# Performance work log

Hardware: AMD Instinct MI355X
Metric: run time of the kernel (lower is better)

The kernel has to match this reference:

```python
import jax, jax.numpy as jnp
import numpy as np

B, LQ, LA, H = 32, 1024, 1024, 512
NEG = -1e7


def setup_inputs() -> dict:
    key = jax.random.key(0)
    kq, ka, ku = jax.random.split(key, 3)
    q = jax.random.normal(kq, (B, LQ, H), dtype=jnp.float32)
    a = jax.random.normal(ka, (B, LA, H), dtype=jnp.float32)
    U = 0.02 * jax.random.normal(ku, (H, H), dtype=jnp.float32)  # init.normal(std=0.02)
    q_mask = jnp.ones((B, LQ, 1), dtype=jnp.float32)
    a_mask = jnp.ones((B, LA, 1), dtype=jnp.float32)
    return {"q": q, "a": a, "U": U, "q_mask": q_mask, "a_mask": a_mask}


def reference(q, a, U, q_mask, a_mask):
    # mask[b,i,j] = q_mask[b,i] * a_mask[b,j]  (nonzero => valid)
    mask = jnp.matmul(q_mask, jnp.swapaxes(a_mask, 1, 2)) > 0  # [B,LQ,LA] bool
    # bilinear score X = q @ U @ a^T
    qU = jnp.einsum('bqh,hk->bqk', q, U)
    X = jnp.einsum('bqk,bak->bqa', qU, a)  # [B,LQ,LA]
    X = jnp.where(mask, X, NEG)
    I = jax.nn.sigmoid(X)
    att_a2q = jnp.max(jax.nn.softmax(I, axis=-1), axis=-1)  # [B,LQ]
    att_q2a = jnp.max(jax.nn.softmax(I, axis=-2), axis=-2)  # [B,LA]
    q_attn = jnp.einsum('blh,bl->bh', q, att_a2q)  # [B,H]
    a_attn = jnp.einsum('blh,bl->bh', a, att_q2a)  # [B,H]
    return q_attn, a_attn
```

## Files before the change

kernel.cpp:

```cpp
#include <hip/hip_runtime.h>

typedef __attribute__((ext_vector_type(8))) short bf16x8;
typedef __attribute__((ext_vector_type(4))) float f32x4;
typedef unsigned short u16;
typedef unsigned int u32;

#define NLOG2E -1.44269504088896f
#define LOG2E   1.44269504088896f
#define SLICE 32768

__device__ __forceinline__ float bf2f(u16 x) {
  union { u32 u; float f; } v; v.u = ((u32)x) << 16; return v.f;
}
__device__ __forceinline__ u16 f2b(float f) {
  union { float f; u32 u; } v; v.f = f;
  return (u16)((v.u + 0x7FFFu + ((v.u >> 16) & 1u)) >> 16);
}
__device__ __forceinline__ u32 pk2(float lo, float hi) {
  return (u32)f2b(lo) | ((u32)f2b(hi) << 16);
}
__device__ __forceinline__ bool inputs_are_bf16(const void* qmask) {
  return *(const u32*)qmask == 0x3F803F80u;
}

__global__ __launch_bounds__(256) void prep_all(
    const void* __restrict__ q, const void* __restrict__ a,
    const void* __restrict__ U, const void* __restrict__ qmask,
    u16* __restrict__ qb, u16* __restrict__ ab, u16* __restrict__ Ut,
    float* __restrict__ out)
{
  const bool bf = inputs_are_bf16(qmask);
  const int t = threadIdx.x;
  if (blockIdx.x < 8192) {
    const bool isq = blockIdx.x < 4096;
    const int idx = (isq ? blockIdx.x : blockIdx.x - 4096) * 256 + t;
    const void* src = isq ? q : a;
    u16* dst = isq ? qb : ab;
    if (bf) {
      const bf16x8* s = (const bf16x8*)src;
      bf16x8* d = (bf16x8*)dst;
      d[idx * 2]     = s[idx * 2];
      d[idx * 2 + 1] = s[idx * 2 + 1];
    } else {
      const float4* s = (const float4*)src + (size_t)idx * 4;
      float4 v0 = s[0], v1 = s[1], v2 = s[2], v3 = s[3];
      uint4* d = (uint4*)dst + (size_t)idx * 2;
      uint4 w0, w1;
      w0.x = pk2(v0.x, v0.y); w0.y = pk2(v0.z, v0.w);
      w0.z = pk2(v1.x, v1.y); w0.w = pk2(v1.z, v1.w);
      w1.x = pk2(v2.x, v2.y); w1.y = pk2(v2.z, v2.w);
      w1.z = pk2(v3.x, v3.y); w1.w = pk2(v3.z, v3.w);
      d[0] = w0;
      d[1] = w1;
    }
  } else {
    const int bb = blockIdx.x - 8192;
    out[bb * 512 + t] = 0.f;
    out[bb * 512 + 256 + t] = 0.f;
    __shared__ u16 tile[64][65];
    const int bx = bb & 7, by = bb >> 3;
    #pragma unroll
    for (int i = 0; i < 16; i++) {
      int r = i * 4 + (t >> 6);
      int c = t & 63;
      size_t gi = (size_t)(by * 64 + r) * 512 + bx * 64 + c;
      tile[c][r] = bf ? ((const u16*)U)[gi] : f2b(((const float*)U)[gi]);
    }
    __syncthreads();
    #pragma unroll
    for (int i = 0; i < 16; i++) {
      int r = i * 4 + (t >> 6);
      int c = t & 63;
      Ut[(size_t)(bx * 64 + r) * 512 + by * 64 + c] = tile[r][c];
    }
  }
}

template<int EPI>
__global__ __launch_bounds__(256, 2) void gemm_bt(
    const u16* __restrict__ A, const u16* __restrict__ B,
    u16* __restrict__ C, float scaleC,
    size_t strideA, size_t strideB,
    const void* __restrict__ q_mask, const void* __restrict__ a_mask,
    float* __restrict__ statsP)
{
  __shared__ __align__(16) char smem[66560];
  u16* As0 = (u16*)smem;
  u16* Bs0 = (u16*)(smem + 16384);
  u16* As1 = (u16*)(smem + 32768);
  u16* Bs1 = (u16*)(smem + 49152);
  u16* Ct  = (u16*)smem;
  float* redS = (float*)smem;
  float* redM = (float*)(smem + 16896);
  float* colS = (float*)(smem + 33792);
  float* colM = (float*)(smem + 34816);
  float* qp = (float*)(smem + 65536);
  float* ap = (float*)(smem + 66048);

  const int bx = blockIdx.x, by = blockIdx.y, bz = blockIdx.z;
  const int tid  = threadIdx.x;
  const int lane = tid & 63;
  const int wave = tid >> 6;
  const int wr = wave >> 1, wc = wave & 1;
  const int l15 = lane & 15, lq = lane >> 4;
  const int rsub = lane >> 3;
  const int csw  = (lane & 7) ^ rsub;

  const u16* Ab = A + strideA * bz + (size_t)by * 128 * 512;
  const u16* Bb = B + strideB * bz + (size_t)bx * 128 * 512;

  if (EPI) {
    const bool bf = inputs_are_bf16(q_mask);
    if (tid < 128) {
      int gi = bz * 1024 + by * 128 + tid;
      float v = bf ? bf2f(((const u16*)q_mask)[gi]) : ((const float*)q_mask)[gi];
      qp[tid] = (v > 0.f) ? 0.f : 1e30f;
    } else {
      int gj = bz * 1024 + bx * 128 + (tid - 128);
      float v = bf ? bf2f(((const u16*)a_mask)[gj]) : ((const float*)a_mask)[gj];
      ap[tid - 128] = (v > 0.f) ? 0.f : 1e30f;
    }
    __syncthreads();
  }

  f32x4 acc[4][4];
  if (EPI) {
    #pragma unroll
    for (int mt = 0; mt < 4; mt++)
      #pragma unroll
      for (int nt = 0; nt < 4; nt++) {
        float cp = ap[wc * 64 + nt * 16 + l15];
        #pragma unroll
        for (int r = 0; r < 4; r++)
          acc[mt][nt][r] = qp[wr * 64 + mt * 16 + lq * 4 + r] + cp;
      }
  } else {
    #pragma unroll
    for (int i = 0; i < 4; i++)
      #pragma unroll
      for (int j = 0; j < 4; j++) {
        f32x4 z = {0.f, 0.f, 0.f, 0.f};
        acc[i][j] = z;
      }
  }

  auto stage = [&](u16* Asb, u16* Bsb, int k0) {
    #pragma unroll
    for (int i = 0; i < 4; i++) {
      const int r0 = wave * 32 + i * 8;
      const size_t go = (size_t)(r0 + rsub) * 512 + k0 + csw * 8;
      __builtin_amdgcn_global_load_lds(
          (const __attribute__((address_space(1))) void*)(Ab + go),
          (__attribute__((address_space(3))) void*)&Asb[r0 * 64], 16, 0, 0);
      __builtin_amdgcn_global_load_lds(
          (const __attribute__((address_space(1))) void*)(Bb + go),
          (__attribute__((address_space(3))) void*)&Bsb[r0 * 64], 16, 0, 0);
    }
  };

  stage(As0, Bs0, 0);
  #pragma unroll
  for (int t = 0; t < 8; t++) {
    u16* Asc = (t & 1) ? As1 : As0;
    u16* Bsc = (t & 1) ? Bs1 : Bs0;
    if (t < 7) {
      stage((t & 1) ? As0 : As1, (t & 1) ? Bs0 : Bs1, (t + 1) * 64);
      asm volatile("s_waitcnt vmcnt(8)\n\ts_barrier" ::: "memory");
    } else {
      asm volatile("s_waitcnt vmcnt(0)\n\ts_barrier" ::: "memory");
    }
    #pragma unroll
    for (int ks = 0; ks < 64; ks += 32) {
      const int cx = ((ks >> 3) + lq) ^ (l15 & 7);
      bf16x8 af[4], bfr[4];
      #pragma unroll
      for (int tt = 0; tt < 4; tt++) {
        af[tt]  = *(const bf16x8*)&Asc[(wr * 64 + tt * 16 + l15) * 64 + cx * 8];
        bfr[tt] = *(const bf16x8*)&Bsc[(wc * 64 + tt * 16 + l15) * 64 + cx * 8];
      }
      #pragma unroll
      for (int mt = 0; mt < 4; mt++)
        #pragma unroll
        for (int nt = 0; nt < 4; nt++)
          acc[mt][nt] = __builtin_amdgcn_mfma_f32_16x16x32_bf16(af[mt], bfr[nt], acc[mt][nt], 0, 0, 0);
    }
    asm volatile("s_waitcnt lgkmcnt(0)\n\ts_barrier" ::: "memory");
  }

  if (!EPI) {
    #pragma unroll
    for (int mt = 0; mt < 4; mt++)
      #pragma unroll
      for (int nt = 0; nt < 4; nt++)
        #pragma unroll
        for (int r = 0; r < 4; r++) {
          int row = wr * 64 + mt * 16 + lq * 4 + r;
          int col = wc * 64 + nt * 16 + l15;
          Ct[row * 144 + col] = f2b(scaleC * acc[mt][nt][r]);
        }
    __syncthreads();
    u16* Cb = C + (size_t)by * 128 * 512 + bx * 128;
    #pragma unroll
    for (int i = 0; i < 8; i++) {
      int c = tid + i * 256;
      int row = c >> 4, cc = c & 15;
      *(bf16x8*)&Cb[(size_t)row * 512 + cc * 8] = *(const bf16x8*)&Ct[row * 144 + cc * 8];
    }
  } else {
    const int gi0 = bz * 1024 + by * 128;
    const int gj0 = bz * 1024 + bx * 128;
    float* rowsumP = statsP + 0      + bx * SLICE;
    float* colsumP = statsP + 262144 + by * SLICE;
    float* rowminP = statsP + 524288 + bx * SLICE;
    float* colminP = statsP + 786432 + by * SLICE;

    float csum[4] = {0.f, 0.f, 0.f, 0.f};
    float cmin[4] = {3e38f, 3e38f, 3e38f, 3e38f};
    #pragma unroll
    for (int mt = 0; mt < 4; mt++) {
      #pragma unroll
      for (int r = 0; r < 4; r++) {
        const int row = wr * 64 + mt * 16 + lq * 4 + r;
        float rsm = 0.f, rmn = 3e38f;
        #pragma unroll
        for (int nt = 0; nt < 4; nt++) {
          float y = acc[mt][nt][r];
          float u = __builtin_amdgcn_exp2f(y);
          float s = __builtin_amdgcn_rcpf(1.f + u);
          float e = __builtin_amdgcn_exp2f(LOG2E * s);
          rsm += e;
          csum[nt] += e;
          rmn = fminf(rmn, y);
          cmin[nt] = fminf(cmin[nt], y);
        }
        redS[row * 33 + l15 + 16 * wc] = rsm;
        redM[row * 33 + l15 + 16 * wc] = rmn;
      }
    }
    #pragma unroll
    for (int nt = 0; nt < 4; nt++) {
      float cs = csum[nt], cm = cmin[nt];
      cs += __shfl_xor(cs, 16); cm = fminf(cm, __shfl_xor(cm, 16));
      cs += __shfl_xor(cs, 32); cm = fminf(cm, __shfl_xor(cm, 32));
      if (lane < 16) {
        int j = wc * 64 + nt * 16 + l15;
        colS[j * 2 + wr] = cs;
        colM[j * 2 + wr] = cm;
      }
    }
    __syncthreads();
    if (tid < 128) {
      float s = 0.f;
      #pragma unroll
      for (int j = 0; j < 32; j++) s += redS[tid * 33 + j];
      rowsumP[gi0 + tid] = s;
      colsumP[gj0 + tid] = colS[tid * 2] + colS[tid * 2 + 1];
    } else {
      const int r = tid - 128;
      float m = 3e38f;
      #pragma unroll
      for (int j = 0; j < 32; j++) m = fminf(m, redM[r * 33 + j]);
      rowminP[gi0 + r] = m;
      colminP[gj0 + r] = fminf(colM[r * 2], colM[r * 2 + 1]);
    }
  }
}

__global__ __launch_bounds__(256) void partial_kernel(
    const u16* __restrict__ qb, const u16* __restrict__ ab,
    const float* __restrict__ statsP, float* __restrict__ out)
{
  __shared__ float att[128];
  const int tid = threadIdx.x;
  const int seg = blockIdx.x;
  const int b = blockIdx.y >> 1, half = blockIdx.y & 1;
  if (tid < 128) {
    const int g = b * 1024 + seg * 128 + tid;
    const float* sumP = statsP + half * 262144;
    const float* minP = statsP + 524288 + half * 262144;
    float s = 0.f, m = 3e38f;
    #pragma unroll
    for (int s8 = 0; s8 < 8; s8++) {
      s += sumP[s8 * SLICE + g];
      m = fminf(m, minP[s8 * SLICE + g]);
    }
    float Imax = __builtin_amdgcn_rcpf(1.f + __builtin_amdgcn_exp2f(m));
    att[tid] = __expf(Imax) * __builtin_amdgcn_rcpf(s);
  }
  __syncthreads();
  const u32* src = (const u32*)((half ? ab : qb) + (size_t)b * 524288
                                + (size_t)seg * 128 * 512);
  float a0 = 0.f, a1 = 0.f;
  #pragma unroll 8
  for (int i = 0; i < 128; i++) {
    u32 w = src[i * 256 + tid];
    float wt = att[i];
    a0 = fmaf(__uint_as_float(w << 16), wt, a0);
    a1 = fmaf(__uint_as_float(w & 0xFFFF0000u), wt, a1);
  }
  float* ob = out + half * 16384 + b * 512 + tid * 2;
  atomicAdd(&ob[0], a0);
  atomicAdd(&ob[1], a1);
}

extern "C" void kernel_launch(void* const* d_in, const int* in_sizes, int n_in,
                              void* d_out, int out_size, void* d_ws, size_t ws_size,
                              hipStream_t stream) {
  const void* q  = d_in[0];
  const void* a  = d_in[1];
  const void* U  = d_in[2];
  const void* qm = d_in[3];
  const void* am = d_in[4];
  float* out = (float*)d_out;

  char* ws = (char*)d_ws;
  u16* qb    = (u16*)ws;
  u16* ab    = (u16*)(ws + 33554432);
  u16* qU    = (u16*)(ws + 67108864);
  u16* Ut    = (u16*)(ws + 100663296);
  float* statsP = (float*)(ws + 100663296);

  prep_all<<<dim3(8256), dim3(256), 0, stream>>>(q, a, U, qm, qb, ab, Ut, out);
  gemm_bt<0><<<dim3(4, 256, 1), dim3(256), 0, stream>>>(
      qb, Ut, qU, NLOG2E, (size_t)0, (size_t)0, qm, am, statsP);
  gemm_bt<1><<<dim3(8, 8, 32), dim3(256), 0, stream>>>(
      qU, ab, (u16*)nullptr, 1.f, (size_t)524288, (size_t)524288, qm, am, statsP);
  partial_kernel<<<dim3(8, 64), dim3(256), 0, stream>>>(qb, ab, statsP, out);
}
```

Baseline: 252.5 us.

## Switch GEMM main loop to 4-stage K=32 LDS pipeline

The GEMM K-loop now uses four LDS buffers of K=32 slices with three loads in flight, replacing the two-buffer K=64 scheme. Each buffer gets a new XOR swizzle for the 32-wide rows. The goal is to hide more global-to-LDS latency behind the MFMA work. The cost is a barrier every 32 K instead of every 64, and the whole 64KB smem region is now used for staging.

```diff
diff --git a/kernel.cpp b/kernel.cpp
--- a/kernel.cpp
+++ b/kernel.cpp
@@ -85,10 +85,6 @@
     float* __restrict__ statsP)
 {
   __shared__ __align__(16) char smem[66560];
-  u16* As0 = (u16*)smem;
-  u16* Bs0 = (u16*)(smem + 16384);
-  u16* As1 = (u16*)(smem + 32768);
-  u16* Bs1 = (u16*)(smem + 49152);
   u16* Ct  = (u16*)smem;
   float* redS = (float*)smem;
   float* redM = (float*)(smem + 16896);
@@ -103,8 +99,11 @@
   const int wave = tid >> 6;
   const int wr = wave >> 1, wc = wave & 1;
   const int l15 = lane & 15, lq = lane >> 4;
-  const int rsub = lane >> 3;
-  const int csw  = (lane & 7) ^ rsub;
+
+  const int srl  = lane >> 2;
+  const int sc   = (lane & 3) ^ ((lane >> 3) & 3);
+  const size_t sgo = (size_t)srl * 512 + sc * 8;
+  const int foff = ((lq ^ ((l15 >> 1) & 3)) * 8);
 
   const u16* Ab = A + strideA * bz + (size_t)by * 128 * 512;
   const u16* Bb = B + strideB * bz + (size_t)bx * 128 * 512;
@@ -144,46 +143,46 @@
       }
   }
 
-  auto stage = [&](u16* Asb, u16* Bsb, int k0) {
-    #pragma unroll
-    for (int i = 0; i < 4; i++) {
-      const int r0 = wave * 32 + i * 8;
-      const size_t go = (size_t)(r0 + rsub) * 512 + k0 + csw * 8;
+  auto stage32 = [&](int buf, int k0) {
+    char* base = smem + buf * 16384;
+    #pragma unroll
+    for (int i = 0; i < 2; i++) {
+      const size_t go = (size_t)(wave * 32 + i * 16) * 512 + k0 + sgo;
       __builtin_amdgcn_global_load_lds(
           (const __attribute__((address_space(1))) void*)(Ab + go),
-          (__attribute__((address_space(3))) void*)&Asb[r0 * 64], 16, 0, 0);
+          (__attribute__((address_space(3))) void*)(base + wave * 2048 + i * 1024), 16, 0, 0);
       __builtin_amdgcn_global_load_lds(
           (const __attribute__((address_space(1))) void*)(Bb + go),
-          (__attribute__((address_space(3))) void*)&Bsb[r0 * 64], 16, 0, 0);
+          (__attribute__((address_space(3))) void*)(base + 8192 + wave * 2048 + i * 1024), 16, 0, 0);
     }
   };
 
-  stage(As0, Bs0, 0);
+  stage32(0, 0);
+  stage32(1, 32);
+  stage32(2, 64);
   #pragma unroll
-  for (int t = 0; t < 8; t++) {
-    u16* Asc = (t & 1) ? As1 : As0;
-    u16* Bsc = (t & 1) ? Bs1 : Bs0;
-    if (t < 7) {
-      stage((t & 1) ? As0 : As1, (t & 1) ? Bs0 : Bs1, (t + 1) * 64);
-      asm volatile("s_waitcnt vmcnt(8)\n\ts_barrier" ::: "memory");
-    } else {
-      asm volatile("s_waitcnt vmcnt(0)\n\ts_barrier" ::: "memory");
-    }
-    #pragma unroll
-    for (int ks = 0; ks < 64; ks += 32) {
-      const int cx = ((ks >> 3) + lq) ^ (l15 & 7);
-      bf16x8 af[4], bfr[4];
-      #pragma unroll
-      for (int tt = 0; tt < 4; tt++) {
-        af[tt]  = *(const bf16x8*)&Asc[(wr * 64 + tt * 16 + l15) * 64 + cx * 8];
-        bfr[tt] = *(const bf16x8*)&Bsc[(wc * 64 + tt * 16 + l15) * 64 + cx * 8];
-      }
-      #pragma unroll
-      for (int mt = 0; mt < 4; mt++)
-        #pragma unroll
-        for (int nt = 0; nt < 4; nt++)
-          acc[mt][nt] = __builtin_amdgcn_mfma_f32_16x16x32_bf16(af[mt], bfr[nt], acc[mt][nt], 0, 0, 0);
-    }
+  for (int t = 0; t < 16; t++) {
+    if (t + 3 < 16) stage32((t + 3) & 3, (t + 3) * 32);
+    if (t < 13)      asm volatile("s_waitcnt vmcnt(12)\n\ts_barrier" ::: "memory");
+    else if (t == 13) asm volatile("s_waitcnt vmcnt(8)\n\ts_barrier" ::: "memory");
+    else if (t == 14) asm volatile("s_waitcnt vmcnt(4)\n\ts_barrier" ::: "memory");
+    else              asm volatile("s_waitcnt vmcnt(0)\n\ts_barrier" ::: "memory");
+
+    const u16* As = (const u16*)(smem + (t & 3) * 16384);
+    const u16* Bs = (const u16*)(smem + (t & 3) * 16384 + 8192);
+    bf16x8 af[4], bfr[4];
+    #pragma unroll
+    for (int tt = 0; tt < 4; tt++) {
+      const int ar = wr * 64 + tt * 16 + l15;
+      const int br = wc * 64 + tt * 16 + l15;
+      af[tt]  = *(const bf16x8*)&As[ar * 32 + foff];
+      bfr[tt] = *(const bf16x8*)&Bs[br * 32 + foff];
+    }
+    #pragma unroll
+    for (int mt = 0; mt < 4; mt++)
+      #pragma unroll
+      for (int nt = 0; nt < 4; nt++)
+        acc[mt][nt] = __builtin_amdgcn_mfma_f32_16x16x32_bf16(af[mt], bfr[nt], acc[mt][nt], 0, 0, 0);
     asm volatile("s_waitcnt lgkmcnt(0)\n\ts_barrier" ::: "memory");
   }
 
```

Result: no change. 250.7 us (-0.7%).
